# Optimization experiments

Hardware: AMD Instinct MI355X
Metric: run time of the kernel (lower is better)

The kernel has to match this reference:

```python
import jax, jax.numpy as jnp
import numpy as np

B, CIN, COUT, K, H, W = 4, 16, 16, 3, 128, 128


def setup_inputs() -> dict:
    key = jax.random.key(0)
    k1, k2, k3 = jax.random.split(key, 3)
    x = jax.random.normal(k1, (B, CIN, H, W), dtype=jnp.float32)
    # kaiming_uniform_(a=1.0): bound = sqrt(6 / ((1 + a^2) * fan_in)), fan_in = Cin*k*k
    fan_in = CIN * K * K
    bound = float(np.sqrt(6.0 / (2.0 * fan_in)))
    weights = jax.random.uniform(k2, (H, W, COUT, CIN, K, K), dtype=jnp.float32,
                                 minval=-bound, maxval=bound)
    bias = jax.random.normal(k3, (H, W, COUT), dtype=jnp.float32)
    return {"x": x, "weights": weights, "bias": bias}


def _xonv2d(x, weights, bias):
    b, c, h, w = x.shape
    k = weights.shape[-1]
    pad = k // 2
    if k % 2 == 1:
        xp = jnp.pad(x, ((0, 0), (0, 0), (pad, pad), (pad, pad)))
    else:
        xp = jnp.pad(x, ((0, 0), (0, 0), (pad - 1, pad), (pad - 1, pad)))
    # Unfold: patch element order matches torch view -> (c, kh, kw) flattened.
    # Stack k*k shifted views: (B, C, k*k, H, W)
    shifts = [xp[:, :, i:i + h, j:j + w] for i in range(k) for j in range(k)]
    patches = jnp.stack(shifts, axis=2)
    wflat = weights.reshape(h, w, weights.shape[2], c, k * k)  # (H,W,O,C,p)
    # out[b,o,h,w] = sum_{c,p} patches[b,c,p,h,w] * wflat[h,w,o,c,p]
    out = jnp.einsum('bcphw,hwocp->bohw', patches, wflat)
    out = out + jnp.transpose(bias, (2, 0, 1))[None]  # (1,O,H,W)
    return out


def reference(x, weights, bias):
    return _xonv2d(x, weights, bias)
```

## Files before the change

### kernel.cpp

```cpp
#include <hip/hip_runtime.h>


#define HWD  128
#define CIND 16
#define COUTD 16
#define BATCH 4

__global__ __launch_bounds__(256) void xonv2d_kernel(
    const float* __restrict__ x,
    const float* __restrict__ wts,
    const float* __restrict__ bias,
    float* __restrict__ out)
{
    const int lane = threadIdx.x & 63;
    const int wave = threadIdx.x >> 6;
    const int site = blockIdx.x * 4 + wave;
    const int h = site >> 7;
    const int w = site & 127;

    const int o = lane & 15;
    const int g = lane >> 4;
    const int c0 = g * 4;

    const float4* wp = (const float4*)(wts + (size_t)site * (COUTD * CIND * 9)
                                           + o * (CIND * 9) + g * 36);
    float4 wv[9];
    #pragma unroll
    for (int i = 0; i < 9; ++i) wv[i] = wp[i];
    const float* wf = (const float*)wv;

    float acc[BATCH] = {0.f, 0.f, 0.f, 0.f};

    const bool interior = (h >= 1) & (h <= HWD - 2) & (w >= 1) & (w <= HWD - 2);

    if (interior) {
        #pragma unroll
        for (int cc = 0; cc < 4; ++cc) {
            const float* xc = x + ((size_t)(c0 + cc) * HWD + (h - 1)) * HWD + (w - 1);
            #pragma unroll
            for (int b = 0; b < BATCH; ++b) {
                const float* xb = xc + (size_t)b * (CIND * HWD * HWD);
                #pragma unroll
                for (int kh = 0; kh < 3; ++kh) {
                    #pragma unroll
                    for (int kw = 0; kw < 3; ++kw) {
                        acc[b] = fmaf(xb[kh * HWD + kw], wf[cc * 9 + kh * 3 + kw], acc[b]);
                    }
                }
            }
        }
    } else {
        #pragma unroll
        for (int cc = 0; cc < 4; ++cc) {
            #pragma unroll
            for (int b = 0; b < BATCH; ++b) {
                const float* xb = x + ((size_t)b * CIND + (c0 + cc)) * (HWD * HWD);
                #pragma unroll
                for (int kh = 0; kh < 3; ++kh) {
                    const int hy = h + kh - 1;
                    #pragma unroll
                    for (int kw = 0; kw < 3; ++kw) {
                        const int wx = w + kw - 1;
                        const bool ok = (hy >= 0) & (hy < HWD) & (wx >= 0) & (wx < HWD);
                        const float xv = ok ? xb[hy * HWD + wx] : 0.f;
                        acc[b] = fmaf(xv, wf[cc * 9 + kh * 3 + kw], acc[b]);
                    }
                }
            }
        }
    }

    #pragma unroll
    for (int b = 0; b < BATCH; ++b) {
        float v = acc[b];
        v += __shfl_down(v, 32);
        v += __shfl_down(v, 16);
        acc[b] = v;
    }

    if (g == 0) {
        const float bv = bias[(size_t)site * COUTD + o];
        #pragma unroll
        for (int b = 0; b < BATCH; ++b) {
            out[((size_t)b * COUTD + o) * (HWD * HWD) + h * HWD + w] = acc[b] + bv;
        }
    }
}

extern "C" void kernel_launch(void* const* d_in, const int* in_sizes, int n_in,
                              void* d_out, int out_size, void* d_ws, size_t ws_size,
                              hipStream_t stream) {
    const float* x    = (const float*)d_in[0];
    const float* wts  = (const float*)d_in[1];
    const float* bias = (const float*)d_in[2];
    float* out = (float*)d_out;

    const int blocks = (HWD * HWD) / 4;
    xonv2d_kernel<<<blocks, 256, 0, stream>>>(x, wts, bias, out);
}
```

Before: 232.1 us.

## Remap blocks per XCD, use nontemporal weight loads and vectorized row reads

Blocks are remapped so each of the 8 XCDs handles a contiguous range of 2048 sites, which should improve L2 locality for the shared input rows. Weights are streamed with nontemporal loads because each value is used only once. Interior input rows are read as unaligned 4-wide vectors, so the interior condition now excludes w=126. The bias load is hoisted, and the output store is spread across all four lane groups by using xor shuffles. The XCD remap assumes the hardware dispatches blocks round-robin across 8 XCDs.

Measured after the change: 272.3 us. 17.3% more time.

```diff
diff --git a/kernel.cpp b/kernel.cpp
--- a/kernel.cpp
+++ b/kernel.cpp
@@ -5,6 +5,9 @@
 #define CIND 16
 #define COUTD 16
 #define BATCH 4
+
+typedef float f4  __attribute__((ext_vector_type(4)));
+typedef float f4u __attribute__((ext_vector_type(4), aligned(4)));
 
 __global__ __launch_bounds__(256) void xonv2d_kernel(
     const float* __restrict__ x,
@@ -14,7 +17,10 @@
 {
     const int lane = threadIdx.x & 63;
     const int wave = threadIdx.x >> 6;
-    const int site = blockIdx.x * 4 + wave;
+
+    const int xcd = blockIdx.x & 7;
+    const int idx = blockIdx.x >> 3;
+    const int site = xcd * 2048 + idx * 4 + wave;
     const int h = site >> 7;
     const int w = site & 127;
 
@@ -22,31 +28,38 @@
     const int g = lane >> 4;
     const int c0 = g * 4;
 
-    const float4* wp = (const float4*)(wts + (size_t)site * (COUTD * CIND * 9)
-                                           + o * (CIND * 9) + g * 36);
-    float4 wv[9];
+    const f4* wp = (const f4*)(wts + (size_t)site * (COUTD * CIND * 9)
+                                    + o * (CIND * 9) + g * 36);
+    f4 wv[9];
     #pragma unroll
-    for (int i = 0; i < 9; ++i) wv[i] = wp[i];
+    for (int i = 0; i < 9; ++i) wv[i] = __builtin_nontemporal_load(wp + i);
     const float* wf = (const float*)wv;
+
+    const float bv = bias[(size_t)site * COUTD + o];
 
     float acc[BATCH] = {0.f, 0.f, 0.f, 0.f};
 
-    const bool interior = (h >= 1) & (h <= HWD - 2) & (w >= 1) & (w <= HWD - 2);
+    const bool interior = (h >= 1) & (h <= HWD - 2) & (w >= 1) & (w <= HWD - 3);
 
     if (interior) {
         #pragma unroll
         for (int cc = 0; cc < 4; ++cc) {
-            const float* xc = x + ((size_t)(c0 + cc) * HWD + (h - 1)) * HWD + (w - 1);
             #pragma unroll
             for (int b = 0; b < BATCH; ++b) {
-                const float* xb = xc + (size_t)b * (CIND * HWD * HWD);
-                #pragma unroll
-                for (int kh = 0; kh < 3; ++kh) {
-                    #pragma unroll
-                    for (int kw = 0; kw < 3; ++kw) {
-                        acc[b] = fmaf(xb[kh * HWD + kw], wf[cc * 9 + kh * 3 + kw], acc[b]);
-                    }
-                }
+                const float* xb = x + (((size_t)(b * CIND + c0 + cc) * HWD + (h - 1)) * HWD) + (w - 1);
+                f4 r0 = *(const f4u*)(xb);
+                f4 r1 = *(const f4u*)(xb + HWD);
+                f4 r2 = *(const f4u*)(xb + 2 * HWD);
+                const float* wr = wf + cc * 9;
+                acc[b] = fmaf(r0.x, wr[0], acc[b]);
+                acc[b] = fmaf(r0.y, wr[1], acc[b]);
+                acc[b] = fmaf(r0.z, wr[2], acc[b]);
+                acc[b] = fmaf(r1.x, wr[3], acc[b]);
+                acc[b] = fmaf(r1.y, wr[4], acc[b]);
+                acc[b] = fmaf(r1.z, wr[5], acc[b]);
+                acc[b] = fmaf(r2.x, wr[6], acc[b]);
+                acc[b] = fmaf(r2.y, wr[7], acc[b]);
+                acc[b] = fmaf(r2.z, wr[8], acc[b]);
             }
         }
     } else {
@@ -54,7 +67,7 @@
         for (int cc = 0; cc < 4; ++cc) {
             #pragma unroll
             for (int b = 0; b < BATCH; ++b) {
-                const float* xb = x + ((size_t)b * CIND + (c0 + cc)) * (HWD * HWD);
+                const float* xb = x + ((size_t)(b * CIND + c0 + cc)) * (HWD * HWD);
                 #pragma unroll
                 for (int kh = 0; kh < 3; ++kh) {
                     const int hy = h + kh - 1;
@@ -70,21 +83,17 @@
         }
     }
 
+    float r[BATCH];
     #pragma unroll
     for (int b = 0; b < BATCH; ++b) {
         float v = acc[b];
-        v += __shfl_down(v, 32);
-        v += __shfl_down(v, 16);
-        acc[b] = v;
+        v += __shfl_xor(v, 32);
+        v += __shfl_xor(v, 16);
+        r[b] = v;
     }
 
-    if (g == 0) {
-        const float bv = bias[(size_t)site * COUTD + o];
-        #pragma unroll
-        for (int b = 0; b < BATCH; ++b) {
-            out[((size_t)b * COUTD + o) * (HWD * HWD) + h * HWD + w] = acc[b] + bv;
-        }
-    }
+    const float vout = (g == 0) ? r[0] : (g == 1) ? r[1] : (g == 2) ? r[2] : r[3];
+    out[((size_t)(g * COUTD + o)) * (HWD * HWD) + h * HWD + w] = vout + bv;
 }
 
 extern "C" void kernel_launch(void* const* d_in, const int* in_sizes, int n_in,
```
